# Kernel optimization log

Hardware: AMD Instinct MI355X
Metric: run time of the kernel (lower is better)

## Reference

```python
import jax, jax.numpy as jnp
import numpy as np

N_NODES = 50000
N_EDGES = 800000
IN_F = 256
HEADS = 4
C = 32  # out_features // heads = 128 // 4
OUT_F = HEADS * C
NEG_SLOPE = 0.2
BN_EPS = 1e-5


def setup_inputs() -> dict:
    key = jax.random.key(0)
    ks = jax.random.split(key, 6)
    x = jax.random.normal(ks[0], (N_NODES, IN_F), dtype=jnp.float32)
    edge_index = jax.random.randint(ks[1], (2, N_EDGES), 0, N_NODES, dtype=jnp.int64)
    W = jax.random.normal(ks[2], (IN_F, OUT_F), dtype=jnp.float32) * 0.05
    att_src = jax.random.normal(ks[3], (HEADS, C), dtype=jnp.float32) * 0.05
    att_dst = jax.random.normal(ks[4], (HEADS, C), dtype=jnp.float32) * 0.05
    bias = jnp.zeros((OUT_F,), dtype=jnp.float32)
    gamma = jnp.ones((OUT_F,), dtype=jnp.float32)
    beta = jnp.zeros((OUT_F,), dtype=jnp.float32)
    return {"x": x, "edge_index": edge_index, "W": W, "att_src": att_src,
            "att_dst": att_dst, "bias": bias, "gamma": gamma, "beta": beta}


def reference(x, edge_index, W, att_src, att_dst, bias, gamma, beta):
    N = x.shape[0]
    # PyG GATConv adds self-loops by default
    loops = jnp.arange(N, dtype=edge_index.dtype)
    src = jnp.concatenate([edge_index[0], loops])  # [E+N]
    dst = jnp.concatenate([edge_index[1], loops])  # [E+N]

    h = (x @ W).reshape(N, HEADS, C)               # [N, H, C]
    a_src = jnp.sum(h * att_src, axis=-1)          # [N, H]
    a_dst = jnp.sum(h * att_dst, axis=-1)          # [N, H]

    e = a_src[src] + a_dst[dst]                    # [E', H]
    e = jax.nn.leaky_relu(e, NEG_SLOPE)
    # segment softmax over destination neighborhoods (self-loops ensure no empty segments)
    e_max = jax.ops.segment_max(e, dst, num_segments=N)
    e = jnp.exp(e - e_max[dst])
    denom = jax.ops.segment_sum(e, dst, num_segments=N)
    alpha = e / (denom[dst] + 1e-16)               # [E', H]

    msg = h[src] * alpha[:, :, None]               # [E', H, C]
    out = jax.ops.segment_sum(msg, dst, num_segments=N).reshape(N, OUT_F) + bias

    # BatchNorm1d in training mode (batch statistics, biased variance)
    mean = jnp.mean(out, axis=0)
    var = jnp.var(out, axis=0)
    out = (out - mean) * jax.lax.rsqrt(var + BN_EPS) * gamma + beta
    # ELU; dropout is identity in eval / deterministic reference
    return jax.nn.elu(out)
```

## Files before the change

kernel.cpp:

```cpp
#include <hip/hip_runtime.h>
#include <hip/hip_fp16.h>
#include <math.h>

#define NN 50000
#define EE 800000
#define EP (EE + NN)
#define INF_ 256
#define OF 128
#define NEG_SLOPE 0.2f
#define BN_EPS 1e-5f
#define NB 196
#define NWIN 8
#define DPW 6250
#define NCH 32
#define QPC 6250

typedef _Float16 half8 __attribute__((ext_vector_type(8)));
typedef float floatx4 __attribute__((ext_vector_type(4)));
typedef int intx4 __attribute__((ext_vector_type(4)));

__global__ __launch_bounds__(256) void k_wprep(const float* __restrict__ W, _Float16* __restrict__ wfrag)
{
    int idx = blockIdx.x * 256 + threadIdx.x;
    int j   = idx & 7;
    int l   = (idx >> 3) & 63;
    int t   = (idx >> 9) & 7;
    int ksg = idx >> 12;
    int k   = ksg * 32 + ((l >> 4) << 3) + j;
    int col = t * 16 + (l & 15);
    wfrag[idx] = (_Float16)W[k * OF + col];
}

__global__ __launch_bounds__(256) void k_gemm(
    const float* __restrict__ x, const _Float16* __restrict__ wfrag,
    const float* __restrict__ att_s, const float* __restrict__ att_d,
    _Float16* __restrict__ h, float* __restrict__ a_src, float* __restrict__ a_dst)
{
    __shared__ __align__(16) _Float16 smem[8192];
    _Float16* xh = smem;

    const int tid  = threadIdx.x;
    const int l    = tid & 63;
    const int w    = tid >> 6;
    const int row0 = blockIdx.x * 64;
    const int lrow = l & 15;
    const int lk8  = (l >> 4) << 3;

    floatx4 acc[8];
    #pragma unroll
    for (int t = 0; t < 8; ++t) acc[t] = (floatx4){0.f, 0.f, 0.f, 0.f};

    for (int kc = 0; kc < 4; ++kc) {
        __syncthreads();
        #pragma unroll
        for (int it = 0; it < 4; ++it) {
            int i  = tid + (it << 8);
            int r  = i >> 4;
            int c4 = (i & 15) << 2;
            int rr = row0 + r; if (rr >= NN) rr = NN - 1;
            float4 v = *(const float4*)&x[rr * INF_ + (kc << 6) + c4];
            _Float16* p = &xh[r * 72 + c4];
            p[0] = (_Float16)v.x; p[1] = (_Float16)v.y;
            p[2] = (_Float16)v.z; p[3] = (_Float16)v.w;
        }
        __syncthreads();
        #pragma unroll
        for (int ks = 0; ks < 2; ++ks) {
            int ksg = kc * 2 + ks;
            half8 a = *(half8*)&xh[(w * 16 + lrow) * 72 + (ks << 5) + lk8];
            const _Float16* wf = &wfrag[(ksg << 12) + (l << 3)];
            #pragma unroll
            for (int t = 0; t < 8; ++t) {
                half8 b = *(const half8*)&wf[t << 9];
                acc[t] = __builtin_amdgcn_mfma_f32_16x16x32_f16(a, b, acc[t], 0, 0, 0);
            }
        }
    }

    float as_c[8], ad_c[8];
    #pragma unroll
    for (int t = 0; t < 8; ++t) { as_c[t] = att_s[t * 16 + lrow]; ad_c[t] = att_d[t * 16 + lrow]; }
    float my_s = 0.f, my_d = 0.f;
    #pragma unroll
    for (int hh = 0; hh < 4; ++hh) {
        #pragma unroll
        for (int reg = 0; reg < 4; ++reg) {
            float ps = acc[2*hh][reg] * as_c[2*hh] + acc[2*hh+1][reg] * as_c[2*hh+1];
            float pd = acc[2*hh][reg] * ad_c[2*hh] + acc[2*hh+1][reg] * ad_c[2*hh+1];
            ps += __shfl_xor(ps, 1); ps += __shfl_xor(ps, 2); ps += __shfl_xor(ps, 4); ps += __shfl_xor(ps, 8);
            pd += __shfl_xor(pd, 1); pd += __shfl_xor(pd, 2); pd += __shfl_xor(pd, 4); pd += __shfl_xor(pd, 8);
            if (lrow == hh * 4 + reg) { my_s = ps; my_d = pd; }
        }
    }
    {
        int myreg = lrow & 3, myhh = lrow >> 2;
        int myrow = row0 + w * 16 + ((l >> 4) << 2) + myreg;
        if (myrow < NN) { a_src[myrow * 4 + myhh] = my_s; a_dst[myrow * 4 + myhh] = my_d; }
    }

    __syncthreads();
    _Float16* ldso = smem + w * 2048;
    #pragma unroll
    for (int t = 0; t < 8; ++t)
        #pragma unroll
        for (int reg = 0; reg < 4; ++reg)
            ldso[(((l >> 4) << 2) + reg) * 128 + t * 16 + lrow] = (_Float16)acc[t][reg];
    __syncthreads();
    {
        _Float16* gdst = h + (size_t)(row0 + w * 16) * OF;
        #pragma unroll
        for (int q = 0; q < 4; ++q) {
            int off = (q << 9) + (l << 3);
            *(half8*)&gdst[off] = *(half8*)&ldso[off];
        }
    }
}

__global__ __launch_bounds__(1024) void k_winhist(const int* __restrict__ ei, int* __restrict__ counts2)
{
    __shared__ int hist[DPW];
    const int w   = blockIdx.x & 7;
    const int c   = blockIdx.x >> 3;
    const int dlo = w * DPW;
    for (int i = threadIdx.x; i < DPW; i += 1024) hist[i] = 0;
    __syncthreads();
    const int q0 = c * QPC;
    for (int q = q0 + threadIdx.x; q < q0 + QPC; q += 1024) {
        intx4 d4 = __builtin_nontemporal_load(((const intx4*)(ei + EE)) + q);
        int dj[4] = {d4.x, d4.y, d4.z, d4.w};
        #pragma unroll
        for (int j = 0; j < 4; ++j) {
            unsigned d = (unsigned)(dj[j] - dlo);
            if (d < DPW) atomicAdd(&hist[d], 1);
        }
    }
    __syncthreads();
    int* dst = counts2 + c * NN + dlo;
    for (int i = threadIdx.x; i < DPW; i += 1024) dst[i] = hist[i];
}

__global__ __launch_bounds__(256) void k_blocksum(const int* __restrict__ counts2, int* __restrict__ partials)
{
    int i = blockIdx.x * 256 + threadIdx.x;
    int v = 0;
    if (i < NN) {
        v = 1;
        #pragma unroll 8
        for (int c = 0; c < NCH; ++c) v += counts2[c * NN + i];
    }
    v += __shfl_xor(v, 1);  v += __shfl_xor(v, 2);  v += __shfl_xor(v, 4);
    v += __shfl_xor(v, 8);  v += __shfl_xor(v, 16); v += __shfl_xor(v, 32);
    __shared__ int wsum[4];
    if ((threadIdx.x & 63) == 0) wsum[threadIdx.x >> 6] = v;
    __syncthreads();
    if (threadIdx.x == 0) partials[blockIdx.x] = wsum[0] + wsum[1] + wsum[2] + wsum[3];
}

__global__ __launch_bounds__(256) void k_scanpart(int* __restrict__ partials)
{
    __shared__ int sm[256];
    int t = threadIdx.x;
    int v = (t < NB) ? partials[t] : 0;
    sm[t] = v;
    __syncthreads();
    for (int off = 1; off < 256; off <<= 1) {
        int u = (t >= off) ? sm[t - off] : 0;
        __syncthreads();
        sm[t] += u;
        __syncthreads();
    }
    if (t < NB) partials[t] = sm[t] - v;
}

__global__ __launch_bounds__(256) void k_writerows(
    const int* __restrict__ counts2, const int* __restrict__ partials,
    int* __restrict__ row_start, int* __restrict__ csr_src, int* __restrict__ base)
{
    __shared__ int sm[256];
    int t = threadIdx.x;
    int i = blockIdx.x * 256 + t;
    int v = 0;
    if (i < NN) {
        v = 1;
        #pragma unroll 8
        for (int c = 0; c < NCH; ++c) v += counts2[c * NN + i];
    }
    sm[t] = v;
    __syncthreads();
    for (int off = 1; off < 256; off <<= 1) {
        int u = (t >= off) ? sm[t - off] : 0;
        __syncthreads();
        sm[t] += u;
        __syncthreads();
    }
    int excl = partials[blockIdx.x] + sm[t] - v;
    if (i < NN) {
        row_start[i] = excl;
        csr_src[excl] = i;
        int p = excl + 1;
        #pragma unroll 8
        for (int c = 0; c < NCH; ++c) { base[c * NN + i] = p; p += counts2[c * NN + i]; }
    }
    if (i == NN) row_start[NN] = excl;
}

__global__ __launch_bounds__(1024) void k_winfill(
    const int* __restrict__ ei, const int* __restrict__ base, int* __restrict__ csr_src)
{
    __shared__ int pos[DPW];
    const int w   = blockIdx.x & 7;
    const int c   = blockIdx.x >> 3;
    const int dlo = w * DPW;
    for (int i = threadIdx.x; i < DPW; i += 1024) pos[i] = base[c * NN + dlo + i];
    __syncthreads();
    const int q0 = c * QPC;
    for (int q = q0 + threadIdx.x; q < q0 + QPC; q += 1024) {
        intx4 d4 = __builtin_nontemporal_load(((const intx4*)(ei + EE)) + q);
        int idx0 = q << 2;
        int dj[4] = {d4.x, d4.y, d4.z, d4.w};
        #pragma unroll
        for (int j = 0; j < 4; ++j) {
            unsigned d = (unsigned)(dj[j] - dlo);
            if (d < DPW) {
                int p = atomicAdd(&pos[d], 1);
                csr_src[p] = ei[idx0 + j];
            }
        }
    }
}

__global__ __launch_bounds__(256) void k_alpha(
    const int* __restrict__ csr_src, const int* __restrict__ row_start,
    const float* __restrict__ a_src, const float* __restrict__ a_dst,
    _Float16* __restrict__ csr_alpha, float* __restrict__ inv_denom)
{
    int gid = blockIdx.x * 256 + threadIdx.x;
    if (gid >= NN * 4) return;
    int node = gid >> 2;
    int hh   = gid & 3;
    int b = row_start[node];
    int e = row_start[node + 1];
    float ad = a_dst[(node << 2) + hh];
    float sum = 0.f;
    for (int k = b; k < e; ++k) {
        int s = csr_src[k];
        float v = a_src[(s << 2) + hh] + ad;
        v = v > 0.f ? v : NEG_SLOPE * v;
        float xv = expf(v);
        sum += xv;
        csr_alpha[(k << 2) + hh] = (_Float16)xv;
    }
    inv_denom[gid] = 1.0f / (sum + 1e-16f);
}

__global__ __launch_bounds__(256) void k_gather(
    const _Float16* __restrict__ h, const int* __restrict__ csr_src,
    const _Float16* __restrict__ csr_alpha, const int* __restrict__ row_start,
    const float* __restrict__ inv_denom, const float* __restrict__ bias,
    _Float16* __restrict__ outh)
{
    int node = blockIdx.x * 4 + (threadIdx.x >> 6);
    int lane = threadIdx.x & 63;
    int g    = lane >> 4;
    int c    = lane & 15;
    int head = c >> 2;
    int b = row_start[node];
    int e = row_start[node + 1];

    float acc[8] = {};
    for (int k = b; k < e; k += 4) {
        int  kk  = k + g;
        bool act = kk < e;
        int  kc  = act ? kk : b;
        int  s   = csr_src[kc];
        float a  = (float)csr_alpha[(kc << 2) + head];
        if (!act) a = 0.f;
        half8 hv = *(const half8*)&h[(size_t)s * OF + (c << 3)];
        #pragma unroll
        for (int j = 0; j < 8; ++j)
            acc[j] = fmaf(a, (float)hv[j], acc[j]);
    }
    #pragma unroll
    for (int j = 0; j < 8; ++j) {
        acc[j] += __shfl_xor(acc[j], 16);
        acc[j] += __shfl_xor(acc[j], 32);
    }
    if (g == 0) {
        float inv = inv_denom[(node << 2) + head];
        float4 b0 = *(const float4*)&bias[c << 3];
        float4 b1 = *(const float4*)&bias[(c << 3) + 4];
        float bj[8] = {b0.x, b0.y, b0.z, b0.w, b1.x, b1.y, b1.z, b1.w};
        half8 o;
        #pragma unroll
        for (int j = 0; j < 8; ++j)
            o[j] = (_Float16)fmaf(acc[j], inv, bj[j]);
        *(half8*)&outh[(size_t)node * OF + (c << 3)] = o;
    }
}

__global__ __launch_bounds__(256) void k_bnred(
    const _Float16* __restrict__ outh, float* __restrict__ fsum, float* __restrict__ fsumsq)
{
    int f = threadIdx.x & 127;
    int r = blockIdx.x * 2 + (threadIdx.x >> 7);
    float s = 0.f, ss = 0.f;
    for (; r < NN; r += gridDim.x * 2) {
        float v = (float)outh[r * OF + f];
        s += v;
        ss = fmaf(v, v, ss);
    }
    atomicAdd(&fsum[f], s);
    atomicAdd(&fsumsq[f], ss);
}

__global__ void k_bnfin(
    const float* __restrict__ fsum, const float* __restrict__ fsumsq,
    const float* __restrict__ gamma, const float* __restrict__ beta,
    float* __restrict__ scale, float* __restrict__ shift)
{
    int f = threadIdx.x;
    float mean = fsum[f] * (1.0f / NN);
    float var  = fsumsq[f] * (1.0f / NN) - mean * mean;
    float sc   = gamma[f] * rsqrtf(var + BN_EPS);
    scale[f] = sc;
    shift[f] = beta[f] - mean * sc;
}

__global__ __launch_bounds__(256) void k_apply(
    const _Float16* __restrict__ outh, const float* __restrict__ scale,
    const float* __restrict__ shift, float* __restrict__ out)
{
    int i    = blockIdx.x * 256 + threadIdx.x;
    int base = i << 3;
    int f    = base & 127;
    half8 v  = *(const half8*)&outh[base];
    float4 sc0 = *(const float4*)&scale[f];
    float4 sc1 = *(const float4*)&scale[f + 4];
    float4 sh0 = *(const float4*)&shift[f];
    float4 sh1 = *(const float4*)&shift[f + 4];
    float scj[8] = {sc0.x, sc0.y, sc0.z, sc0.w, sc1.x, sc1.y, sc1.z, sc1.w};
    float shj[8] = {sh0.x, sh0.y, sh0.z, sh0.w, sh1.x, sh1.y, sh1.z, sh1.w};
    float r[8];
    #pragma unroll
    for (int j = 0; j < 8; ++j) {
        float t = fmaf((float)v[j], scj[j], shj[j]);
        r[j] = t > 0.f ? t : expm1f(t);
    }
    *(float4*)&out[base]     = make_float4(r[0], r[1], r[2], r[3]);
    *(float4*)&out[base + 4] = make_float4(r[4], r[5], r[6], r[7]);
}

extern "C" void kernel_launch(void* const* d_in, const int* in_sizes, int n_in,
                              void* d_out, int out_size, void* d_ws, size_t ws_size,
                              hipStream_t stream)
{
    const float* x     = (const float*)d_in[0];
    const int*   ei    = (const int*)d_in[1];
    const float* W     = (const float*)d_in[2];
    const float* att_s = (const float*)d_in[3];
    const float* att_d = (const float*)d_in[4];
    const float* bias  = (const float*)d_in[5];
    const float* gamma = (const float*)d_in[6];
    const float* beta  = (const float*)d_in[7];
    float* out = (float*)d_out;

    float* ws           = (float*)d_ws;
    _Float16* h         = (_Float16*)ws;
    _Float16* outh      = (_Float16*)(ws + 3210000);
    float* a_src        = ws + 6410000;
    float* a_dst        = a_src + 200000;
    float* wfrag_f      = a_dst + 200000;
    float* csr_alpha_f  = wfrag_f + 20000;
    float* inv_denom    = csr_alpha_f + 1700000;
    float* fsum         = inv_denom + 200000;
    float* fsumsq       = fsum + 128;
    float* scale        = fsumsq + 128;
    float* shift        = scale + 128;
    int* row_start      = (int*)(shift + 128);
    int* csr_src        = row_start + NN + 1;
    int* partials       = csr_src + EP;
    int* counts2        = (int*)csr_alpha_f;
    int* cbase          = (int*)outh;
    _Float16* wfrag     = (_Float16*)wfrag_f;
    _Float16* csr_alpha = (_Float16*)csr_alpha_f;

    hipMemsetAsync(fsum, 0, 256 * sizeof(float), stream);

    k_wprep<<<128, 256, 0, stream>>>(W, wfrag);
    k_gemm<<<(NN + 63) / 64, 256, 0, stream>>>(x, wfrag, att_s, att_d, h, a_src, a_dst);
    k_winhist<<<NWIN * NCH, 1024, 0, stream>>>(ei, counts2);
    k_blocksum<<<NB, 256, 0, stream>>>(counts2, partials);
    k_scanpart<<<1, 256, 0, stream>>>(partials);
    k_writerows<<<NB, 256, 0, stream>>>(counts2, partials, row_start, csr_src, cbase);
    k_winfill<<<NWIN * NCH, 1024, 0, stream>>>(ei, cbase, csr_src);
    k_alpha<<<(NN * 4 + 255) / 256, 256, 0, stream>>>(csr_src, row_start, a_src, a_dst, csr_alpha, inv_denom);
    k_gather<<<NN / 4, 256, 0, stream>>>(h, csr_src, csr_alpha, row_start, inv_denom, bias, outh);
    k_bnred<<<512, 256, 0, stream>>>(outh, fsum, fsumsq);
    k_bnfin<<<1, 128, 0, stream>>>(fsum, fsumsq, gamma, beta, scale, shift);
    k_apply<<<NN * OF / 8 / 256, 256, 0, stream>>>(outh, scale, shift, out);
}
```

Measured before the change: 173.0 us.

## Fuse attention-logit computation into CSR build and compute softmax denominator in gather

Removes the separate k_alpha kernel. Unnormalized exp(leaky_relu) attention weights are now computed where edges are scattered into CSR: in k_winfill for real edges and in k_writerows for self-loops. The softmax denominator is summed inside k_gather from the alpha values it already reads, so the inv_denom buffer goes away. The fsum memset is folded into k_wprep, and the workspace aliasing of counts2/cbase is moved onto outh. This saves a kernel launch and a full pass over the CSR, but adds scattered a_src/a_dst loads and the exp work to the atomic fill loop.

```diff
diff --git a/kernel.cpp b/kernel.cpp
--- a/kernel.cpp
+++ b/kernel.cpp
@@ -16,12 +16,20 @@
 #define QPC 6250
 
 typedef _Float16 half8 __attribute__((ext_vector_type(8)));
+typedef _Float16 half4 __attribute__((ext_vector_type(4)));
 typedef float floatx4 __attribute__((ext_vector_type(4)));
 typedef int intx4 __attribute__((ext_vector_type(4)));
 
-__global__ __launch_bounds__(256) void k_wprep(const float* __restrict__ W, _Float16* __restrict__ wfrag)
+__device__ __forceinline__ float lrelu_exp(float v) {
+    v = v > 0.f ? v : NEG_SLOPE * v;
+    return expf(v);
+}
+
+__global__ __launch_bounds__(256) void k_wprep(const float* __restrict__ W, _Float16* __restrict__ wfrag,
+                                               float* __restrict__ fsum)
 {
     int idx = blockIdx.x * 256 + threadIdx.x;
+    if (idx < 256) fsum[idx] = 0.f;
     int j   = idx & 7;
     int l   = (idx >> 3) & 63;
     int t   = (idx >> 9) & 7;
@@ -174,7 +182,9 @@
 
 __global__ __launch_bounds__(256) void k_writerows(
     const int* __restrict__ counts2, const int* __restrict__ partials,
-    int* __restrict__ row_start, int* __restrict__ csr_src, int* __restrict__ base)
+    const float* __restrict__ a_src, const float* __restrict__ a_dst,
+    int* __restrict__ row_start, int* __restrict__ csr_src,
+    _Float16* __restrict__ csr_alpha, int* __restrict__ base)
 {
     __shared__ int sm[256];
     int t = threadIdx.x;
@@ -197,6 +207,14 @@
     if (i < NN) {
         row_start[i] = excl;
         csr_src[excl] = i;
+        float4 as = *(const float4*)&a_src[i << 2];
+        float4 ad = *(const float4*)&a_dst[i << 2];
+        half4 al;
+        al[0] = (_Float16)lrelu_exp(as.x + ad.x);
+        al[1] = (_Float16)lrelu_exp(as.y + ad.y);
+        al[2] = (_Float16)lrelu_exp(as.z + ad.z);
+        al[3] = (_Float16)lrelu_exp(as.w + ad.w);
+        *(half4*)&csr_alpha[excl << 2] = al;
         int p = excl + 1;
         #pragma unroll 8
         for (int c = 0; c < NCH; ++c) { base[c * NN + i] = p; p += counts2[c * NN + i]; }
@@ -205,7 +223,9 @@
 }
 
 __global__ __launch_bounds__(1024) void k_winfill(
-    const int* __restrict__ ei, const int* __restrict__ base, int* __restrict__ csr_src)
+    const int* __restrict__ ei, const int* __restrict__ base,
+    const float* __restrict__ a_src, const float* __restrict__ a_dst,
+    int* __restrict__ csr_src, _Float16* __restrict__ csr_alpha)
 {
     __shared__ int pos[DPW];
     const int w   = blockIdx.x & 7;
@@ -222,42 +242,26 @@
         for (int j = 0; j < 4; ++j) {
             unsigned d = (unsigned)(dj[j] - dlo);
             if (d < DPW) {
+                int s = ei[idx0 + j];
                 int p = atomicAdd(&pos[d], 1);
-                csr_src[p] = ei[idx0 + j];
+                csr_src[p] = s;
+                float4 as = *(const float4*)&a_src[s << 2];
+                float4 ad = *(const float4*)&a_dst[dj[j] << 2];
+                half4 al;
+                al[0] = (_Float16)lrelu_exp(as.x + ad.x);
+                al[1] = (_Float16)lrelu_exp(as.y + ad.y);
+                al[2] = (_Float16)lrelu_exp(as.z + ad.z);
+                al[3] = (_Float16)lrelu_exp(as.w + ad.w);
+                *(half4*)&csr_alpha[p << 2] = al;
             }
         }
     }
-}
-
-__global__ __launch_bounds__(256) void k_alpha(
-    const int* __restrict__ csr_src, const int* __restrict__ row_start,
-    const float* __restrict__ a_src, const float* __restrict__ a_dst,
-    _Float16* __restrict__ csr_alpha, float* __restrict__ inv_denom)
-{
-    int gid = blockIdx.x * 256 + threadIdx.x;
-    if (gid >= NN * 4) return;
-    int node = gid >> 2;
-    int hh   = gid & 3;
-    int b = row_start[node];
-    int e = row_start[node + 1];
-    float ad = a_dst[(node << 2) + hh];
-    float sum = 0.f;
-    for (int k = b; k < e; ++k) {
-        int s = csr_src[k];
-        float v = a_src[(s << 2) + hh] + ad;
-        v = v > 0.f ? v : NEG_SLOPE * v;
-        float xv = expf(v);
-        sum += xv;
-        csr_alpha[(k << 2) + hh] = (_Float16)xv;
-    }
-    inv_denom[gid] = 1.0f / (sum + 1e-16f);
 }
 
 __global__ __launch_bounds__(256) void k_gather(
     const _Float16* __restrict__ h, const int* __restrict__ csr_src,
     const _Float16* __restrict__ csr_alpha, const int* __restrict__ row_start,
-    const float* __restrict__ inv_denom, const float* __restrict__ bias,
-    _Float16* __restrict__ outh)
+    const float* __restrict__ bias, _Float16* __restrict__ outh)
 {
     int node = blockIdx.x * 4 + (threadIdx.x >> 6);
     int lane = threadIdx.x & 63;
@@ -268,6 +272,7 @@
     int e = row_start[node + 1];
 
     float acc[8] = {};
+    float dsum = 0.f;
     for (int k = b; k < e; k += 4) {
         int  kk  = k + g;
         bool act = kk < e;
@@ -275,6 +280,7 @@
         int  s   = csr_src[kc];
         float a  = (float)csr_alpha[(kc << 2) + head];
         if (!act) a = 0.f;
+        dsum += a;
         half8 hv = *(const half8*)&h[(size_t)s * OF + (c << 3)];
         #pragma unroll
         for (int j = 0; j < 8; ++j)
@@ -285,8 +291,10 @@
         acc[j] += __shfl_xor(acc[j], 16);
         acc[j] += __shfl_xor(acc[j], 32);
     }
+    dsum += __shfl_xor(dsum, 16);
+    dsum += __shfl_xor(dsum, 32);
     if (g == 0) {
-        float inv = inv_denom[(node << 2) + head];
+        float inv = 1.0f / (dsum + 1e-16f);
         float4 b0 = *(const float4*)&bias[c << 3];
         float4 b1 = *(const float4*)&bias[(c << 3) + 4];
         float bj[8] = {b0.x, b0.y, b0.z, b0.w, b1.x, b1.y, b1.z, b1.w};
@@ -371,30 +379,26 @@
     float* a_dst        = a_src + 200000;
     float* wfrag_f      = a_dst + 200000;
     float* csr_alpha_f  = wfrag_f + 20000;
-    float* inv_denom    = csr_alpha_f + 1700000;
-    float* fsum         = inv_denom + 200000;
+    float* fsum         = csr_alpha_f + 1700000;
     float* fsumsq       = fsum + 128;
     float* scale        = fsumsq + 128;
     float* shift        = scale + 128;
     int* row_start      = (int*)(shift + 128);
     int* csr_src        = row_start + NN + 1;
     int* partials       = csr_src + EP;
-    int* counts2        = (int*)csr_alpha_f;
-    int* cbase          = (int*)outh;
+    int* counts2        = (int*)outh;
+    int* cbase          = counts2 + NCH * NN;
     _Float16* wfrag     = (_Float16*)wfrag_f;
     _Float16* csr_alpha = (_Float16*)csr_alpha_f;
 
-    hipMemsetAsync(fsum, 0, 256 * sizeof(float), stream);
-
-    k_wprep<<<128, 256, 0, stream>>>(W, wfrag);
+    k_wprep<<<128, 256, 0, stream>>>(W, wfrag, fsum);
     k_gemm<<<(NN + 63) / 64, 256, 0, stream>>>(x, wfrag, att_s, att_d, h, a_src, a_dst);
     k_winhist<<<NWIN * NCH, 1024, 0, stream>>>(ei, counts2);
     k_blocksum<<<NB, 256, 0, stream>>>(counts2, partials);
     k_scanpart<<<1, 256, 0, stream>>>(partials);
-    k_writerows<<<NB, 256, 0, stream>>>(counts2, partials, row_start, csr_src, cbase);
-    k_winfill<<<NWIN * NCH, 1024, 0, stream>>>(ei, cbase, csr_src);
-    k_alpha<<<(NN * 4 + 255) / 256, 256, 0, stream>>>(csr_src, row_start, a_src, a_dst, csr_alpha, inv_denom);
-    k_gather<<<NN / 4, 256, 0, stream>>>(h, csr_src, csr_alpha, row_start, inv_denom, bias, outh);
+    k_writerows<<<NB, 256, 0, stream>>>(counts2, partials, a_src, a_dst, row_start, csr_src, csr_alpha, cbase);
+    k_winfill<<<NWIN * NCH, 1024, 0, stream>>>(ei, cbase, a_src, a_dst, csr_src, csr_alpha);
+    k_gather<<<NN / 4, 256, 0, stream>>>(h, csr_src, csr_alpha, row_start, bias, outh);
     k_bnred<<<512, 256, 0, stream>>>(outh, fsum, fsumsq);
     k_bnfin<<<1, 128, 0, stream>>>(fsum, fsumsq, gamma, beta, scale, shift);
     k_apply<<<NN * OF / 8 / 256, 256, 0, stream>>>(outh, scale, shift, out);
```

Result: slower. 179.7 us (+3.9%).
